# Optimization experiments

Measured on AMD Instinct MI355X. Metric: run time of the kernel, lower is better.

## Reference

```python
import jax, jax.numpy as jnp
import numpy as np

EPS = 1e-5

def _ln(x, w, b):
    mu = jnp.mean(x, axis=-1, keepdims=True)
    var = jnp.var(x, axis=-1, keepdims=True)
    return (x - mu) * jax.lax.rsqrt(var + EPS) * w + b

def setup_inputs() -> dict:
    key = jax.random.key(0)
    ks = jax.random.split(key, 12)
    B, N, CZ, CH = 1, 384, 128, 128
    z = jax.random.normal(ks[0], (B, N, N, CZ), dtype=jnp.float32)
    mask = jnp.ones((B, N, N), dtype=jnp.float32)
    s_z = 1.0 / np.sqrt(CZ)
    s_h = 1.0 / np.sqrt(CH)
    return {
        "z": z,
        "mask": mask,
        "ln_in_w": jnp.ones((CZ,), jnp.float32),
        "ln_in_b": jnp.zeros((CZ,), jnp.float32),
        "w_a_g": jax.random.normal(ks[1], (CZ, CH), jnp.float32) * s_z,
        "b_a_g": jnp.ones((CH,), jnp.float32),
        "w_a_p": jax.random.normal(ks[2], (CZ, CH), jnp.float32) * s_z,
        "b_a_p": jnp.zeros((CH,), jnp.float32),
        "w_b_g": jax.random.normal(ks[3], (CZ, CH), jnp.float32) * s_z,
        "b_b_g": jnp.ones((CH,), jnp.float32),
        "w_b_p": jax.random.normal(ks[4], (CZ, CH), jnp.float32) * s_z,
        "b_b_p": jnp.zeros((CH,), jnp.float32),
        "ln_out_w": jnp.ones((CH,), jnp.float32),
        "ln_out_b": jnp.zeros((CH,), jnp.float32),
        "w_z": jax.random.normal(ks[5], (CH, CZ), jnp.float32) * s_h,
        "b_z": jnp.zeros((CZ,), jnp.float32),
        "w_g": jax.random.normal(ks[6], (CZ, CZ), jnp.float32) * s_z,
        "b_g": jnp.ones((CZ,), jnp.float32),
    }

def reference(z, mask, ln_in_w, ln_in_b, w_a_g, b_a_g, w_a_p, b_a_p,
              w_b_g, b_b_g, w_b_p, b_b_p, ln_out_w, ln_out_b,
              w_z, b_z, w_g, b_g):
    m = mask[..., None]                                   # [B,N,N,1]
    zn = _ln(z, ln_in_w, ln_in_b)                         # [B,N,N,Cz]
    a = m * jax.nn.sigmoid(zn @ w_a_g + b_a_g) * (zn @ w_a_p + b_a_p)
    b = m * jax.nn.sigmoid(zn @ w_b_g + b_b_g) * (zn @ w_b_p + b_b_p)
    # outgoing: p[b,i,j,c] = sum_k a[b,i,k,c] * b[b,j,k,c]
    x = jnp.einsum('bikc,bjkc->bijc', a, b)
    x = _ln(x, ln_out_w, ln_out_b)
    x = (x @ w_z + b_z) * jax.nn.sigmoid(zn @ w_g + b_g)
    return x
```

## Files before the change

### kernel.cpp

```cpp
#include <hip/hip_runtime.h>
#include <hip/hip_bf16.h>

#define NN 384
#define NP (NN*NN)
#define CC 128
#define LDP 136

typedef __attribute__((ext_vector_type(8))) short bf16x8;
typedef __attribute__((ext_vector_type(4))) float f32x4;
typedef __attribute__((ext_vector_type(8))) unsigned short u16x8;

__device__ __forceinline__ unsigned short f2bf(float f){
  unsigned int u = __float_as_uint(f);
  u += 0x7FFFu + ((u >> 16) & 1u);
  return (unsigned short)(u >> 16);
}
__device__ __forceinline__ float bf2f(unsigned short h){
  return __uint_as_float(((unsigned int)h) << 16);
}
__device__ __forceinline__ float sigm(float x){ return 1.f / (1.f + __expf(-x)); }

__device__ __forceinline__ void stage_w_T(const float* __restrict__ W, unsigned short* w_lds, int tid){
  for (int i = tid; i < CC*CC; i += 256){
    int k = i >> 7, n = i & 127;
    w_lds[n*LDP + k] = f2bf(W[i]);
  }
}

__device__ __forceinline__ void gemm_128(const unsigned short* a_lds, const unsigned short* w_lds,
                                         int wave, int lane, f32x4 acc[2][8]){
  const int l16 = lane & 15;
  const int lk  = (lane >> 4) * 8;
  const int row0 = wave * 32;
  #pragma unroll
  for (int kc = 0; kc < 4; ++kc){
    bf16x8 af[2], bfr[8];
    #pragma unroll
    for (int mr = 0; mr < 2; ++mr)
      af[mr] = *(const bf16x8*)&a_lds[(row0 + mr*16 + l16)*LDP + kc*32 + lk];
    #pragma unroll
    for (int nr = 0; nr < 8; ++nr)
      bfr[nr] = *(const bf16x8*)&w_lds[(nr*16 + l16)*LDP + kc*32 + lk];
    #pragma unroll
    for (int mr = 0; mr < 2; ++mr)
      #pragma unroll
      for (int nr = 0; nr < 8; ++nr)
        acc[mr][nr] = __builtin_amdgcn_mfma_f32_16x16x32_bf16(af[mr], bfr[nr], acc[mr][nr], 0, 0, 0);
  }
}

__global__ __launch_bounds__(256) void k1(
    const float* __restrict__ z, const float* __restrict__ mask,
    const float* __restrict__ lnw, const float* __restrict__ lnb,
    const float* __restrict__ wag, const float* __restrict__ bag,
    const float* __restrict__ wap, const float* __restrict__ bap,
    const float* __restrict__ wbg, const float* __restrict__ bbg,
    const float* __restrict__ wbp, const float* __restrict__ bbp,
    const float* __restrict__ wg,  const float* __restrict__ bgt,
    unsigned short* __restrict__ At, unsigned short* __restrict__ Bt,
    unsigned short* __restrict__ G)
{
  __shared__ unsigned short zn[CC*LDP];
  __shared__ unsigned short wl[CC*LDP];
  const int tid = threadIdx.x;
  const int wave = tid >> 6, lane = tid & 63;
  const int posbase = blockIdx.x * 128;

  float lw0 = lnw[lane], lw1 = lnw[lane+64];
  float lb0 = lnb[lane], lb1 = lnb[lane+64];
  for (int it = 0; it < 32; ++it){
    int pl = wave*32 + it;
    size_t base = (size_t)(posbase + pl) * CC;
    float v0 = z[base + lane], v1 = z[base + lane + 64];
    float s = v0 + v1, q = v0*v0 + v1*v1;
    #pragma unroll
    for (int off = 32; off; off >>= 1){ s += __shfl_xor(s, off); q += __shfl_xor(q, off); }
    float mean = s * (1.f/128.f);
    float rstd = rsqrtf(q*(1.f/128.f) - mean*mean + 1e-5f);
    zn[pl*LDP + lane]      = f2bf((v0 - mean)*rstd*lw0 + lb0);
    zn[pl*LDP + lane + 64] = f2bf((v1 - mean)*rstd*lw1 + lb1);
  }
  __syncthreads();

  for (int pr = 0; pr < 2; ++pr){
    const float* Wg  = pr ? wbg : wag;
    const float* Wp  = pr ? wbp : wap;
    const float* Bg_ = pr ? bbg : bag;
    const float* Bp_ = pr ? bbp : bap;
    unsigned short* dst = pr ? Bt : At;

    stage_w_T(Wg, wl, tid);
    __syncthreads();
    f32x4 accg[2][8] = {};
    gemm_128(zn, wl, wave, lane, accg);
    __syncthreads();
    stage_w_T(Wp, wl, tid);
    __syncthreads();
    f32x4 accp[2][8] = {};
    gemm_128(zn, wl, wave, lane, accp);
    __syncthreads();

    const int l16 = lane & 15;
    #pragma unroll
    for (int nr = 0; nr < 8; ++nr){
      int c = nr*16 + l16;
      float bgv = Bg_[c], bpv = Bp_[c];
      #pragma unroll
      for (int mr = 0; mr < 2; ++mr){
        #pragma unroll
        for (int r = 0; r < 4; ++r){
          int pl = wave*32 + mr*16 + (lane>>4)*4 + r;
          float m = mask[posbase + pl];
          float v = m * sigm(accg[mr][nr][r] + bgv) * (accp[mr][nr][r] + bpv);
          wl[c*LDP + pl] = f2bf(v);
        }
      }
    }
    __syncthreads();
    for (int i = tid; i < CC*16; i += 256){
      int c = i >> 4, seg = i & 15;
      u16x8 v = *(const u16x8*)&wl[c*LDP + seg*8];
      *(u16x8*)&dst[(size_t)c*NP + posbase + seg*8] = v;
    }
    __syncthreads();
  }

  stage_w_T(wg, wl, tid);
  __syncthreads();
  f32x4 accG[2][8] = {};
  gemm_128(zn, wl, wave, lane, accG);
  __syncthreads();
  {
    const int l16 = lane & 15;
    #pragma unroll
    for (int nr = 0; nr < 8; ++nr){
      int c = nr*16 + l16;
      float bgv = bgt[c];
      #pragma unroll
      for (int mr = 0; mr < 2; ++mr)
        #pragma unroll
        for (int r = 0; r < 4; ++r){
          int pl = wave*32 + mr*16 + (lane>>4)*4 + r;
          wl[pl*LDP + c] = f2bf(sigm(accG[mr][nr][r] + bgv));
        }
    }
  }
  __syncthreads();
  for (int i = tid; i < CC*16; i += 256){
    int pl = i >> 4, seg = i & 15;
    u16x8 v = *(const u16x8*)&wl[pl*LDP + seg*8];
    *(u16x8*)&G[((size_t)(posbase + pl))*CC + seg*8] = v;
  }
}

__global__ __launch_bounds__(256) void k2(const unsigned short* __restrict__ At,
                                          const unsigned short* __restrict__ Bt,
                                          unsigned short* __restrict__ Xt)
{
  __shared__ unsigned short As[128*64];
  __shared__ unsigned short Bs[128*64];
  const int c  = blockIdx.y;
  const int ti = blockIdx.x / 3, tj = blockIdx.x % 3;
  const int tid = threadIdx.x, wave = tid >> 6, lane = tid & 63;
  const unsigned short* Ag = At + (size_t)c*NP + (size_t)(ti*128)*NN;
  const unsigned short* Bg = Bt + (size_t)c*NP + (size_t)(tj*128)*NN;
  const int l16 = lane & 15, lk = (lane >> 4)*8, row0 = wave*32;
  f32x4 acc[2][8] = {};
  for (int k0 = 0; k0 < NN; k0 += 64){
    __syncthreads();
    for (int i = tid; i < 1024; i += 256){
      int row = i >> 3, seg = i & 7;
      *(u16x8*)&As[row*64 + seg*8] = *(const u16x8*)&Ag[(size_t)row*NN + k0 + seg*8];
      *(u16x8*)&Bs[row*64 + seg*8] = *(const u16x8*)&Bg[(size_t)row*NN + k0 + seg*8];
    }
    __syncthreads();
    #pragma unroll
    for (int kc = 0; kc < 2; ++kc){
      bf16x8 af[2], bfr[8];
      #pragma unroll
      for (int mr = 0; mr < 2; ++mr)
        af[mr] = *(const bf16x8*)&As[(row0 + mr*16 + l16)*64 + kc*32 + lk];
      #pragma unroll
      for (int nr = 0; nr < 8; ++nr)
        bfr[nr] = *(const bf16x8*)&Bs[(nr*16 + l16)*64 + kc*32 + lk];
      #pragma unroll
      for (int mr = 0; mr < 2; ++mr)
        #pragma unroll
        for (int nr = 0; nr < 8; ++nr)
          acc[mr][nr] = __builtin_amdgcn_mfma_f32_16x16x32_bf16(af[mr], bfr[nr], acc[mr][nr], 0,0,0);
    }
  }
  size_t base = (size_t)c*NP + (size_t)(ti*128)*NN + tj*128;
  #pragma unroll
  for (int mr = 0; mr < 2; ++mr)
    #pragma unroll
    for (int nr = 0; nr < 8; ++nr)
      #pragma unroll
      for (int r = 0; r < 4; ++r){
        int row = row0 + mr*16 + (lane>>4)*4 + r;
        int col = nr*16 + l16;
        Xt[base + (size_t)row*NN + col] = f2bf(acc[mr][nr][r]);
      }
}

__global__ __launch_bounds__(256) void k3(const unsigned short* __restrict__ Xt,
                                          const unsigned short* __restrict__ G,
                                          const float* __restrict__ lnw, const float* __restrict__ lnb,
                                          const float* __restrict__ wz, const float* __restrict__ bz,
                                          float* __restrict__ out)
{
  __shared__ unsigned short xc[CC*LDP];
  __shared__ unsigned short yl[CC*LDP];
  __shared__ unsigned short wl[CC*LDP];
  const int tid = threadIdx.x, wave = tid >> 6, lane = tid & 63;
  const int posbase = blockIdx.x * 128;

  for (int i = tid; i < CC*16; i += 256){
    int cch = i >> 4, seg = i & 15;
    *(u16x8*)&xc[cch*LDP + seg*8] = *(const u16x8*)&Xt[(size_t)cch*NP + posbase + seg*8];
  }
  stage_w_T(wz, wl, tid);
  __syncthreads();

  float lw0 = lnw[lane], lw1 = lnw[lane+64];
  float lb0 = lnb[lane], lb1 = lnb[lane+64];
  for (int it = 0; it < 32; ++it){
    int pl = wave*32 + it;
    float v0 = bf2f(xc[lane*LDP + pl]);
    float v1 = bf2f(xc[(lane+64)*LDP + pl]);
    float s = v0 + v1, q = v0*v0 + v1*v1;
    #pragma unroll
    for (int off = 32; off; off >>= 1){ s += __shfl_xor(s, off); q += __shfl_xor(q, off); }
    float mean = s*(1.f/128.f);
    float rstd = rsqrtf(q*(1.f/128.f) - mean*mean + 1e-5f);
    yl[pl*LDP + lane]    = f2bf((v0 - mean)*rstd*lw0 + lb0);
    yl[pl*LDP + lane+64] = f2bf((v1 - mean)*rstd*lw1 + lb1);
  }
  __syncthreads();

  f32x4 acc[2][8] = {};
  gemm_128(yl, wl, wave, lane, acc);

  const int l16 = lane & 15;
  #pragma unroll
  for (int nr = 0; nr < 8; ++nr){
    int cch = nr*16 + l16;
    float bzv = bz[cch];
    #pragma unroll
    for (int mr = 0; mr < 2; ++mr)
      #pragma unroll
      for (int r = 0; r < 4; ++r){
        int pl = wave*32 + mr*16 + (lane>>4)*4 + r;
        size_t o = (size_t)(posbase + pl)*CC + cch;
        out[o] = (acc[mr][nr][r] + bzv) * bf2f(G[o]);
      }
  }
}

extern "C" void kernel_launch(void* const* d_in, const int* in_sizes, int n_in,
                              void* d_out, int out_size, void* d_ws, size_t ws_size,
                              hipStream_t stream)
{
  const float* z    = (const float*)d_in[0];
  const float* mask = (const float*)d_in[1];
  const float* lniw = (const float*)d_in[2];
  const float* lnib = (const float*)d_in[3];
  const float* wag  = (const float*)d_in[4];
  const float* bag  = (const float*)d_in[5];
  const float* wap  = (const float*)d_in[6];
  const float* bap  = (const float*)d_in[7];
  const float* wbg  = (const float*)d_in[8];
  const float* bbg  = (const float*)d_in[9];
  const float* wbp  = (const float*)d_in[10];
  const float* bbp  = (const float*)d_in[11];
  const float* lnow = (const float*)d_in[12];
  const float* lnob = (const float*)d_in[13];
  const float* wz   = (const float*)d_in[14];
  const float* bz   = (const float*)d_in[15];
  const float* wg   = (const float*)d_in[16];
  const float* bg   = (const float*)d_in[17];
  float* out = (float*)d_out;

  unsigned short* At = (unsigned short*)d_ws;
  unsigned short* Bt = At + (size_t)CC*NP;
  unsigned short* G  = Bt + (size_t)CC*NP;
  unsigned short* Xt = G  + (size_t)CC*NP;

  k1<<<dim3(NP/128), 256, 0, stream>>>(z, mask, lniw, lnib, wag, bag, wap, bap,
                                       wbg, bbg, wbp, bbp, wg, bg, At, Bt, G);
  k2<<<dim3(9, CC), 256, 0, stream>>>(At, Bt, Xt);
  k3<<<dim3(NP/128), 256, 0, stream>>>(Xt, G, lnow, lnob, wz, bz, out);
}
```

Measured before the change: 487.7 us.

## Pre-convert weights once, read them from global, swizzle LDS, reduce LDS footprint

Adds a small kernel that converts and transposes all six weight matrices to bf16 once per call, so the per-block kernels read weight fragments directly from global/L2 instead of restaging each weight into LDS with scalar stores. LDS padding is replaced by XOR swizzles, and k1 drops its second 34KB buffer, which raises occupancy and removes several barriers. The A/B projection now writes channel-major output directly from registers, and the output LayerNorm in k3 is restructured into a stats pass plus a normalize-and-transpose pass. The costs are scattered 2-byte global stores in k1, extra global traffic for weight fragments, and one more launch.

```diff
diff --git a/kernel.cpp b/kernel.cpp
--- a/kernel.cpp
+++ b/kernel.cpp
@@ -4,11 +4,14 @@
 #define NN 384
 #define NP (NN*NN)
 #define CC 128
-#define LDP 136
 
 typedef __attribute__((ext_vector_type(8))) short bf16x8;
 typedef __attribute__((ext_vector_type(4))) float f32x4;
 typedef __attribute__((ext_vector_type(8))) unsigned short u16x8;
+typedef __attribute__((ext_vector_type(4))) unsigned short u16x4;
+
+#define SW16(row, col) ((col) ^ (((row)&15)<<3))
+#define SW8(row, col)  ((col) ^ (((row)&7)<<3))
 
 __device__ __forceinline__ unsigned short f2bf(float f){
   unsigned int u = __float_as_uint(f);
@@ -20,136 +23,156 @@
 }
 __device__ __forceinline__ float sigm(float x){ return 1.f / (1.f + __expf(-x)); }
 
-__device__ __forceinline__ void stage_w_T(const float* __restrict__ W, unsigned short* w_lds, int tid){
-  for (int i = tid; i < CC*CC; i += 256){
+__global__ __launch_bounds__(256) void k0(const float* __restrict__ w0, const float* __restrict__ w1,
+                                          const float* __restrict__ w2, const float* __restrict__ w3,
+                                          const float* __restrict__ w4, const float* __restrict__ w5,
+                                          unsigned short* __restrict__ Wt)
+{
+  __shared__ unsigned short t[CC*CC];
+  const float* W = blockIdx.x==0?w0: blockIdx.x==1?w1: blockIdx.x==2?w2:
+                   blockIdx.x==3?w3: blockIdx.x==4?w4: w5;
+  unsigned short* o = Wt + blockIdx.x*CC*CC;
+  for (int i = threadIdx.x; i < CC*CC; i += 256){
     int k = i >> 7, n = i & 127;
-    w_lds[n*LDP + k] = f2bf(W[i]);
-  }
-}
-
-__device__ __forceinline__ void gemm_128(const unsigned short* a_lds, const unsigned short* w_lds,
-                                         int wave, int lane, f32x4 acc[2][8]){
-  const int l16 = lane & 15;
-  const int lk  = (lane >> 4) * 8;
-  const int row0 = wave * 32;
-  #pragma unroll
-  for (int kc = 0; kc < 4; ++kc){
-    bf16x8 af[2], bfr[8];
-    #pragma unroll
-    for (int mr = 0; mr < 2; ++mr)
-      af[mr] = *(const bf16x8*)&a_lds[(row0 + mr*16 + l16)*LDP + kc*32 + lk];
-    #pragma unroll
-    for (int nr = 0; nr < 8; ++nr)
-      bfr[nr] = *(const bf16x8*)&w_lds[(nr*16 + l16)*LDP + kc*32 + lk];
-    #pragma unroll
-    for (int mr = 0; mr < 2; ++mr)
-      #pragma unroll
-      for (int nr = 0; nr < 8; ++nr)
-        acc[mr][nr] = __builtin_amdgcn_mfma_f32_16x16x32_bf16(af[mr], bfr[nr], acc[mr][nr], 0, 0, 0);
+    t[n*CC + SW16(n, k)] = f2bf(W[i]);
+  }
+  __syncthreads();
+  for (int i = threadIdx.x; i < CC*16; i += 256){
+    int n = i >> 4, g = i & 15;
+    *(u16x8*)&o[n*CC + g*8] = *(const u16x8*)&t[n*CC + SW16(n, g*8)];
   }
 }
 
 __global__ __launch_bounds__(256) void k1(
     const float* __restrict__ z, const float* __restrict__ mask,
     const float* __restrict__ lnw, const float* __restrict__ lnb,
-    const float* __restrict__ wag, const float* __restrict__ bag,
-    const float* __restrict__ wap, const float* __restrict__ bap,
-    const float* __restrict__ wbg, const float* __restrict__ bbg,
-    const float* __restrict__ wbp, const float* __restrict__ bbp,
-    const float* __restrict__ wg,  const float* __restrict__ bgt,
+    const float* __restrict__ bag, const float* __restrict__ bap,
+    const float* __restrict__ bbg, const float* __restrict__ bbp,
+    const float* __restrict__ bgt,
+    const unsigned short* __restrict__ Wt,
     unsigned short* __restrict__ At, unsigned short* __restrict__ Bt,
     unsigned short* __restrict__ G)
 {
-  __shared__ unsigned short zn[CC*LDP];
-  __shared__ unsigned short wl[CC*LDP];
-  const int tid = threadIdx.x;
-  const int wave = tid >> 6, lane = tid & 63;
-  const int posbase = blockIdx.x * 128;
-
-  float lw0 = lnw[lane], lw1 = lnw[lane+64];
-  float lb0 = lnb[lane], lb1 = lnb[lane+64];
-  for (int it = 0; it < 32; ++it){
-    int pl = wave*32 + it;
-    size_t base = (size_t)(posbase + pl) * CC;
-    float v0 = z[base + lane], v1 = z[base + lane + 64];
-    float s = v0 + v1, q = v0*v0 + v1*v1;
-    #pragma unroll
-    for (int off = 32; off; off >>= 1){ s += __shfl_xor(s, off); q += __shfl_xor(q, off); }
-    float mean = s * (1.f/128.f);
-    float rstd = rsqrtf(q*(1.f/128.f) - mean*mean + 1e-5f);
-    zn[pl*LDP + lane]      = f2bf((v0 - mean)*rstd*lw0 + lb0);
-    zn[pl*LDP + lane + 64] = f2bf((v1 - mean)*rstd*lw1 + lb1);
-  }
-  __syncthreads();
-
+  __shared__ unsigned short zn[CC*CC];
+  const int tid = threadIdx.x, wave = tid>>6, lane = tid&63;
+  const int l16 = lane&15, lg = lane>>4;
+  const int posbase = blockIdx.x*128;
+
+  {
+    const int lh = lane&31, hh = lane>>5;
+    const float4 lw4 = *(const float4*)&lnw[4*lh];
+    const float4 lb4 = *(const float4*)&lnb[4*lh];
+    for (int it = 0; it < 16; ++it){
+      int pl = wave*32 + it*2 + hh;
+      float4 v = *(const float4*)&z[(size_t)(posbase+pl)*CC + 4*lh];
+      float s = v.x+v.y+v.z+v.w;
+      float q = v.x*v.x+v.y*v.y+v.z*v.z+v.w*v.w;
+      #pragma unroll
+      for (int off = 16; off; off >>= 1){ s += __shfl_xor(s, off); q += __shfl_xor(q, off); }
+      float mean = s*(1.f/128.f);
+      float rstd = rsqrtf(q*(1.f/128.f) - mean*mean + 1e-5f);
+      u16x4 o;
+      o[0] = f2bf((v.x-mean)*rstd*lw4.x + lb4.x);
+      o[1] = f2bf((v.y-mean)*rstd*lw4.y + lb4.y);
+      o[2] = f2bf((v.z-mean)*rstd*lw4.z + lb4.z);
+      o[3] = f2bf((v.w-mean)*rstd*lw4.w + lb4.w);
+      *(u16x4*)&zn[pl*CC + SW16(pl, 4*lh)] = o;
+    }
+  }
+  __syncthreads();
+
+  #pragma unroll 1
   for (int pr = 0; pr < 2; ++pr){
-    const float* Wg  = pr ? wbg : wag;
-    const float* Wp  = pr ? wbp : wap;
+    const unsigned short* Wg = Wt + (pr*2+0)*CC*CC;
+    const unsigned short* Wp = Wt + (pr*2+1)*CC*CC;
     const float* Bg_ = pr ? bbg : bag;
     const float* Bp_ = pr ? bbp : bap;
     unsigned short* dst = pr ? Bt : At;
-
-    stage_w_T(Wg, wl, tid);
-    __syncthreads();
-    f32x4 accg[2][8] = {};
-    gemm_128(zn, wl, wave, lane, accg);
-    __syncthreads();
-    stage_w_T(Wp, wl, tid);
-    __syncthreads();
-    f32x4 accp[2][8] = {};
-    gemm_128(zn, wl, wave, lane, accp);
-    __syncthreads();
-
-    const int l16 = lane & 15;
+    float4 bg4[2], bp4[2];
+    #pragma unroll
+    for (int ma = 0; ma < 2; ++ma){
+      int cb = wave*32 + ma*16 + lg*4;
+      bg4[ma] = *(const float4*)&Bg_[cb];
+      bp4[ma] = *(const float4*)&Bp_[cb];
+    }
+    #pragma unroll 1
+    for (int half = 0; half < 2; ++half){
+      f32x4 ag[2][4] = {}; f32x4 ap[2][4] = {};
+      #pragma unroll
+      for (int kc = 0; kc < 4; ++kc){
+        const int kb = kc*32 + lg*8;
+        bf16x8 bz[4], wgf[2], wpf[2];
+        #pragma unroll
+        for (int nb = 0; nb < 4; ++nb){
+          int pos = half*64 + nb*16 + l16;
+          bz[nb] = *(const bf16x8*)&zn[pos*CC + SW16(pos, kb)];
+        }
+        #pragma unroll
+        for (int ma = 0; ma < 2; ++ma){
+          int c = wave*32 + ma*16 + l16;
+          wgf[ma] = *(const bf16x8*)&Wg[c*CC + kb];
+          wpf[ma] = *(const bf16x8*)&Wp[c*CC + kb];
+        }
+        #pragma unroll
+        for (int ma = 0; ma < 2; ++ma)
+          #pragma unroll
+          for (int nb = 0; nb < 4; ++nb){
+            ag[ma][nb] = __builtin_amdgcn_mfma_f32_16x16x32_bf16(wgf[ma], bz[nb], ag[ma][nb], 0,0,0);
+            ap[ma][nb] = __builtin_amdgcn_mfma_f32_16x16x32_bf16(wpf[ma], bz[nb], ap[ma][nb], 0,0,0);
+          }
+      }
+      #pragma unroll
+      for (int nb = 0; nb < 4; ++nb){
+        int pos = posbase + half*64 + nb*16 + l16;
+        float m = mask[pos];
+        #pragma unroll
+        for (int ma = 0; ma < 2; ++ma){
+          int cb = wave*32 + ma*16 + lg*4;
+          #pragma unroll
+          for (int r = 0; r < 4; ++r){
+            float bgv = r==0?bg4[ma].x : r==1?bg4[ma].y : r==2?bg4[ma].z : bg4[ma].w;
+            float bpv = r==0?bp4[ma].x : r==1?bp4[ma].y : r==2?bp4[ma].z : bp4[ma].w;
+            float v = m * sigm(ag[ma][nb][r] + bgv) * (ap[ma][nb][r] + bpv);
+            dst[(size_t)(cb + r)*NP + pos] = f2bf(v);
+          }
+        }
+      }
+    }
+  }
+
+  {
+    const unsigned short* Wgt = Wt + 4*CC*CC;
+    f32x4 acc[2][8] = {};
+    #pragma unroll
+    for (int kc = 0; kc < 4; ++kc){
+      const int kb = kc*32 + lg*8;
+      bf16x8 az[2], wf[8];
+      #pragma unroll
+      for (int ma = 0; ma < 2; ++ma){
+        int pos = wave*32 + ma*16 + l16;
+        az[ma] = *(const bf16x8*)&zn[pos*CC + SW16(pos, kb)];
+      }
+      #pragma unroll
+      for (int nr = 0; nr < 8; ++nr)
+        wf[nr] = *(const bf16x8*)&Wgt[(nr*16+l16)*CC + kb];
+      #pragma unroll
+      for (int ma = 0; ma < 2; ++ma)
+        #pragma unroll
+        for (int nr = 0; nr < 8; ++nr)
+          acc[ma][nr] = __builtin_amdgcn_mfma_f32_16x16x32_bf16(az[ma], wf[nr], acc[ma][nr], 0,0,0);
+    }
     #pragma unroll
     for (int nr = 0; nr < 8; ++nr){
       int c = nr*16 + l16;
-      float bgv = Bg_[c], bpv = Bp_[c];
-      #pragma unroll
-      for (int mr = 0; mr < 2; ++mr){
+      float bv = bgt[c];
+      #pragma unroll
+      for (int ma = 0; ma < 2; ++ma)
         #pragma unroll
         for (int r = 0; r < 4; ++r){
-          int pl = wave*32 + mr*16 + (lane>>4)*4 + r;
-          float m = mask[posbase + pl];
-          float v = m * sigm(accg[mr][nr][r] + bgv) * (accp[mr][nr][r] + bpv);
-          wl[c*LDP + pl] = f2bf(v);
+          int pos = posbase + wave*32 + ma*16 + lg*4 + r;
+          G[(size_t)pos*CC + c] = f2bf(sigm(acc[ma][nr][r] + bv));
         }
-      }
-    }
-    __syncthreads();
-    for (int i = tid; i < CC*16; i += 256){
-      int c = i >> 4, seg = i & 15;
-      u16x8 v = *(const u16x8*)&wl[c*LDP + seg*8];
-      *(u16x8*)&dst[(size_t)c*NP + posbase + seg*8] = v;
-    }
-    __syncthreads();
-  }
-
-  stage_w_T(wg, wl, tid);
-  __syncthreads();
-  f32x4 accG[2][8] = {};
-  gemm_128(zn, wl, wave, lane, accG);
-  __syncthreads();
-  {
-    const int l16 = lane & 15;
-    #pragma unroll
-    for (int nr = 0; nr < 8; ++nr){
-      int c = nr*16 + l16;
-      float bgv = bgt[c];
-      #pragma unroll
-      for (int mr = 0; mr < 2; ++mr)
-        #pragma unroll
-        for (int r = 0; r < 4; ++r){
-          int pl = wave*32 + mr*16 + (lane>>4)*4 + r;
-          wl[pl*LDP + c] = f2bf(sigm(accG[mr][nr][r] + bgv));
-        }
-    }
-  }
-  __syncthreads();
-  for (int i = tid; i < CC*16; i += 256){
-    int pl = i >> 4, seg = i & 15;
-    u16x8 v = *(const u16x8*)&wl[pl*LDP + seg*8];
-    *(u16x8*)&G[((size_t)(posbase + pl))*CC + seg*8] = v;
+    }
   }
 }
 
@@ -162,97 +185,151 @@
   const int c  = blockIdx.y;
   const int ti = blockIdx.x / 3, tj = blockIdx.x % 3;
   const int tid = threadIdx.x, wave = tid >> 6, lane = tid & 63;
+  const int l16 = lane & 15, lg = lane >> 4;
   const unsigned short* Ag = At + (size_t)c*NP + (size_t)(ti*128)*NN;
   const unsigned short* Bg = Bt + (size_t)c*NP + (size_t)(tj*128)*NN;
-  const int l16 = lane & 15, lk = (lane >> 4)*8, row0 = wave*32;
   f32x4 acc[2][8] = {};
   for (int k0 = 0; k0 < NN; k0 += 64){
     __syncthreads();
-    for (int i = tid; i < 1024; i += 256){
-      int row = i >> 3, seg = i & 7;
-      *(u16x8*)&As[row*64 + seg*8] = *(const u16x8*)&Ag[(size_t)row*NN + k0 + seg*8];
-      *(u16x8*)&Bs[row*64 + seg*8] = *(const u16x8*)&Bg[(size_t)row*NN + k0 + seg*8];
+    #pragma unroll
+    for (int it = 0; it < 4; ++it){
+      int i = tid + it*256;
+      int row = i >> 3, g = i & 7;
+      u16x8 va = *(const u16x8*)&Ag[(size_t)row*NN + k0 + g*8];
+      u16x8 vb = *(const u16x8*)&Bg[(size_t)row*NN + k0 + g*8];
+      *(u16x8*)&As[row*64 + SW8(row, g*8)] = va;
+      *(u16x8*)&Bs[row*64 + SW8(row, g*8)] = vb;
     }
     __syncthreads();
     #pragma unroll
     for (int kc = 0; kc < 2; ++kc){
+      const int kb = kc*32 + lg*8;
       bf16x8 af[2], bfr[8];
       #pragma unroll
-      for (int mr = 0; mr < 2; ++mr)
-        af[mr] = *(const bf16x8*)&As[(row0 + mr*16 + l16)*64 + kc*32 + lk];
-      #pragma unroll
-      for (int nr = 0; nr < 8; ++nr)
-        bfr[nr] = *(const bf16x8*)&Bs[(nr*16 + l16)*64 + kc*32 + lk];
-      #pragma unroll
-      for (int mr = 0; mr < 2; ++mr)
+      for (int ma = 0; ma < 2; ++ma){
+        int row = wave*32 + ma*16 + l16;
+        af[ma] = *(const bf16x8*)&As[row*64 + SW8(row, kb)];
+      }
+      #pragma unroll
+      for (int nr = 0; nr < 8; ++nr){
+        int row = nr*16 + l16;
+        bfr[nr] = *(const bf16x8*)&Bs[row*64 + SW8(row, kb)];
+      }
+      #pragma unroll
+      for (int ma = 0; ma < 2; ++ma)
         #pragma unroll
         for (int nr = 0; nr < 8; ++nr)
-          acc[mr][nr] = __builtin_amdgcn_mfma_f32_16x16x32_bf16(af[mr], bfr[nr], acc[mr][nr], 0,0,0);
+          acc[ma][nr] = __builtin_amdgcn_mfma_f32_16x16x32_bf16(af[ma], bfr[nr], acc[ma][nr], 0,0,0);
     }
   }
   size_t base = (size_t)c*NP + (size_t)(ti*128)*NN + tj*128;
   #pragma unroll
-  for (int mr = 0; mr < 2; ++mr)
+  for (int ma = 0; ma < 2; ++ma)
     #pragma unroll
     for (int nr = 0; nr < 8; ++nr)
       #pragma unroll
       for (int r = 0; r < 4; ++r){
-        int row = row0 + mr*16 + (lane>>4)*4 + r;
+        int row = wave*32 + ma*16 + lg*4 + r;
         int col = nr*16 + l16;
-        Xt[base + (size_t)row*NN + col] = f2bf(acc[mr][nr][r]);
+        Xt[base + (size_t)row*NN + col] = f2bf(acc[ma][nr][r]);
       }
 }
 
 __global__ __launch_bounds__(256) void k3(const unsigned short* __restrict__ Xt,
                                           const unsigned short* __restrict__ G,
                                           const float* __restrict__ lnw, const float* __restrict__ lnb,
-                                          const float* __restrict__ wz, const float* __restrict__ bz,
+                                          const unsigned short* __restrict__ Wzt, const float* __restrict__ bz,
                                           float* __restrict__ out)
 {
-  __shared__ unsigned short xc[CC*LDP];
-  __shared__ unsigned short yl[CC*LDP];
-  __shared__ unsigned short wl[CC*LDP];
-  const int tid = threadIdx.x, wave = tid >> 6, lane = tid & 63;
-  const int posbase = blockIdx.x * 128;
-
-  for (int i = tid; i < CC*16; i += 256){
-    int cch = i >> 4, seg = i & 15;
-    *(u16x8*)&xc[cch*LDP + seg*8] = *(const u16x8*)&Xt[(size_t)cch*NP + posbase + seg*8];
-  }
-  stage_w_T(wz, wl, tid);
-  __syncthreads();
-
-  float lw0 = lnw[lane], lw1 = lnw[lane+64];
-  float lb0 = lnb[lane], lb1 = lnb[lane+64];
-  for (int it = 0; it < 32; ++it){
-    int pl = wave*32 + it;
-    float v0 = bf2f(xc[lane*LDP + pl]);
-    float v1 = bf2f(xc[(lane+64)*LDP + pl]);
-    float s = v0 + v1, q = v0*v0 + v1*v1;
-    #pragma unroll
-    for (int off = 32; off; off >>= 1){ s += __shfl_xor(s, off); q += __shfl_xor(q, off); }
-    float mean = s*(1.f/128.f);
-    float rstd = rsqrtf(q*(1.f/128.f) - mean*mean + 1e-5f);
-    yl[pl*LDP + lane]    = f2bf((v0 - mean)*rstd*lw0 + lb0);
-    yl[pl*LDP + lane+64] = f2bf((v1 - mean)*rstd*lw1 + lb1);
+  __shared__ unsigned short xc[CC*CC];
+  __shared__ unsigned short yt[CC*CC];
+  __shared__ float mu[CC], rs[CC];
+  const int tid = threadIdx.x, wave = tid>>6, lane = tid&63;
+  const int l16 = lane&15, lg = lane>>4;
+  const int posbase = blockIdx.x*128;
+
+  #pragma unroll
+  for (int it = 0; it < 8; ++it){
+    int i = tid + it*256;
+    int cc = i >> 4, g = i & 15;
+    u16x8 v = *(const u16x8*)&Xt[(size_t)cc*NP + posbase + g*8];
+    *(u16x8*)&xc[cc*CC + SW16(cc, g*8)] = v;
+  }
+  __syncthreads();
+
+  {
+    const int lh = lane&31, hh = lane>>5;
+    f32x4 s4 = {0,0,0,0}, q4 = {0,0,0,0};
+    for (int ci = 0; ci < 64; ++ci){
+      int cc = hh*64 + ci;
+      u16x4 v = *(const u16x4*)&xc[cc*CC + SW16(cc, 4*lh)];
+      #pragma unroll
+      for (int j = 0; j < 4; ++j){
+        float f = bf2f(v[j]);
+        s4[j] += f; q4[j] += f*f;
+      }
+    }
+    #pragma unroll
+    for (int j = 0; j < 4; ++j){ s4[j] += __shfl_xor(s4[j], 32); q4[j] += __shfl_xor(q4[j], 32); }
+    if (hh == 0){
+      f32x4 m4, r4;
+      #pragma unroll
+      for (int j = 0; j < 4; ++j){
+        float mean = s4[j]*(1.f/128.f);
+        m4[j] = mean;
+        r4[j] = rsqrtf(q4[j]*(1.f/128.f) - mean*mean + 1e-5f);
+      }
+      *(f32x4*)&mu[4*lh] = m4;
+      *(f32x4*)&rs[4*lh] = r4;
+    }
+  }
+  __syncthreads();
+
+  #pragma unroll
+  for (int it = 0; it < 8; ++it){
+    int i = tid + it*256;
+    int cc = i & 127, g = i >> 7;
+    u16x8 v = *(const u16x8*)&xc[cc*CC + SW16(cc, g*8)];
+    float lw = lnw[cc], lb = lnb[cc];
+    #pragma unroll
+    for (int j = 0; j < 8; ++j){
+      int pos = g*8 + j;
+      float f = (bf2f(v[j]) - mu[pos]) * rs[pos] * lw + lb;
+      yt[pos*CC + SW16(pos, cc)] = f2bf(f);
+    }
   }
   __syncthreads();
 
   f32x4 acc[2][8] = {};
-  gemm_128(yl, wl, wave, lane, acc);
-
-  const int l16 = lane & 15;
+  #pragma unroll
+  for (int kc = 0; kc < 4; ++kc){
+    const int kb = kc*32 + lg*8;
+    bf16x8 af[2], wf[8];
+    #pragma unroll
+    for (int ma = 0; ma < 2; ++ma){
+      int pos = wave*32 + ma*16 + l16;
+      af[ma] = *(const bf16x8*)&yt[pos*CC + SW16(pos, kb)];
+    }
+    #pragma unroll
+    for (int nr = 0; nr < 8; ++nr)
+      wf[nr] = *(const bf16x8*)&Wzt[(nr*16+l16)*CC + kb];
+    #pragma unroll
+    for (int ma = 0; ma < 2; ++ma)
+      #pragma unroll
+      for (int nr = 0; nr < 8; ++nr)
+        acc[ma][nr] = __builtin_amdgcn_mfma_f32_16x16x32_bf16(af[ma], wf[nr], acc[ma][nr], 0,0,0);
+  }
   #pragma unroll
   for (int nr = 0; nr < 8; ++nr){
     int cch = nr*16 + l16;
     float bzv = bz[cch];
     #pragma unroll
-    for (int mr = 0; mr < 2; ++mr)
+    for (int ma = 0; ma < 2; ++ma)
       #pragma unroll
       for (int r = 0; r < 4; ++r){
-        int pl = wave*32 + mr*16 + (lane>>4)*4 + r;
-        size_t o = (size_t)(posbase + pl)*CC + cch;
-        out[o] = (acc[mr][nr][r] + bzv) * bf2f(G[o]);
+        int pos = posbase + wave*32 + ma*16 + lg*4 + r;
+        size_t o = (size_t)pos*CC + cch;
+        out[o] = (acc[ma][nr][r] + bzv) * bf2f(G[o]);
       }
   }
 }
@@ -281,13 +358,14 @@
   const float* bg   = (const float*)d_in[17];
   float* out = (float*)d_out;
 
-  unsigned short* At = (unsigned short*)d_ws;
+  unsigned short* Wt = (unsigned short*)d_ws;
+  unsigned short* At = Wt + 6*CC*CC;
   unsigned short* Bt = At + (size_t)CC*NP;
   unsigned short* G  = Bt + (size_t)CC*NP;
   unsigned short* Xt = G  + (size_t)CC*NP;
 
-  k1<<<dim3(NP/128), 256, 0, stream>>>(z, mask, lniw, lnib, wag, bag, wap, bap,
-                                       wbg, bbg, wbp, bbp, wg, bg, At, Bt, G);
+  k0<<<6, 256, 0, stream>>>(wag, wap, wbg, wbp, wg, wz, Wt);
+  k1<<<NP/128, 256, 0, stream>>>(z, mask, lniw, lnib, bag, bap, bbg, bbp, bg, Wt, At, Bt, G);
   k2<<<dim3(9, CC), 256, 0, stream>>>(At, Bt, Xt);
-  k3<<<dim3(NP/128), 256, 0, stream>>>(Xt, G, lnow, lnob, wz, bz, out);
-}
+  k3<<<NP/128, 256, 0, stream>>>(Xt, G, lnow, lnob, Wt + 5*CC*CC, bz, out);
+}
```

Measured after the change: 400.7 us. -17.8%, faster.
